# Performance work log

Hardware: AMD Instinct MI355X
Metric: run time of the kernel (lower is better)

Reference implementation:

```python
import jax, jax.numpy as jnp
import numpy as np

B, T, C = 32, 1024, 1024
N_LAYER, LAYER_ID, FIRST_SA = 12, 3, 1
RWKV_K_CLAMP = 60.0
RWKV_K_EPS = 1e-16


def _init_params():
    # decay_speed init exactly as in RWKV_TimeMix.__init__
    f1 = 3.0 + (LAYER_ID - FIRST_SA) / (N_LAYER - 1 - FIRST_SA) * (1.2 - 3.0)
    f2 = 0.65 + (LAYER_ID - FIRST_SA) / (N_LAYER - 1 - FIRST_SA) * (0.4 - 0.65)
    h = np.arange(C, dtype=np.float64)
    decay_speed = np.power(f2, h / (C - 1) * 7) * f1
    time_decay = np.log(decay_speed).astype(np.float32)          # (C,)
    time_first = np.full((C,), np.log(0.3), dtype=np.float32)     # (C,)
    tm = np.ones((C,), dtype=np.float32)
    tm[: C // 2] = 0.0                                            # time_mix
    return jnp.asarray(time_decay), jnp.asarray(time_first), jnp.asarray(tm)


def setup_inputs() -> dict:
    key = jax.random.key(0)
    ks = jax.random.split(key, 5)
    x = jax.random.normal(ks[0], (B, T, C), dtype=jnp.float32)
    scale = 0.02
    Wk = jax.random.normal(ks[1], (C, C), dtype=jnp.float32) * scale
    Wv = jax.random.normal(ks[2], (C, C), dtype=jnp.float32) * scale
    Wr = jax.random.normal(ks[3], (C, C), dtype=jnp.float32) * scale
    Wo = jax.random.normal(ks[4], (C, C), dtype=jnp.float32) * scale
    time_decay, time_first, time_mix = _init_params()
    return {"x": x, "time_decay": time_decay, "time_first": time_first,
            "time_mix": time_mix, "Wk": Wk, "Wv": Wv, "Wr": Wr, "Wo": Wo}


def _wkv(decay, first_w, y, eps):
    # out[b,t,c] = eps + first_w[c]*y[b,t,c] + sum_{u<t} decay[c]^(t-1-u) * y[b,u,c]
    # computed as a linear recurrence S[t] = decay*S[t-1] + y[t] via associative scan.
    a = jnp.broadcast_to(decay, y.shape)
    def comb(l, r):
        a1, b1 = l
        a2, b2 = r
        return (a1 * a2, a2 * b1 + b2)
    _, S = jax.lax.associative_scan(comb, (a, y), axis=1)
    S_prev = jnp.pad(S, ((0, 0), (1, 0), (0, 0)))[:, :-1]  # S[t-1], S[-1]=0
    return eps + first_w * y + S_prev


def reference(x, time_decay, time_first, time_mix, Wk, Wv, Wr, Wo):
    Bn, Tn, Cn = x.shape
    # time shift: ZeroPad2d((0,0,1,-1)) -> shifted[t] = x[t-1], shifted[0]=0
    xs = jnp.pad(x, ((0, 0), (1, 0), (0, 0)))[:, :-1]
    xm = x * time_mix + xs * (1.0 - time_mix)
    k = xm @ Wk.T
    v = xm @ Wv.T
    r = xm @ Wr.T
    k = jnp.exp(jnp.minimum(k, RWKV_K_CLAMP))
    kv = k * v
    decay = jnp.exp(-jnp.exp(time_decay))   # lag-d weight (d>=1): decay^(d-1)
    first_w = jnp.exp(time_first)           # lag-0 weight
    wkv = _wkv(decay, first_w, kv, 0.0)
    wk = _wkv(decay, first_w, k, RWKV_K_EPS)
    rwkv = jax.nn.sigmoid(r) * (wkv / wk)
    return rwkv @ Wo.T
```

## Files before the change

### kernel.cpp

```cpp
#include <hip/hip_runtime.h>


#define DEV __device__ __forceinline__

constexpr int Bc = 32, Tc = 1024, Cc = 1024;
constexpr int Mdim = Bc * Tc;
constexpr int Ndim = Cc;
constexpr int Kdim = Cc;
constexpr int NT = Kdim / 32;
constexpr int CHUNK = 128;
constexpr int LOOKB = 128;
constexpr int NCH = Tc / CHUNK;

typedef short bf16x8 __attribute__((ext_vector_type(8)));
typedef float f32x4  __attribute__((ext_vector_type(4)));

DEV unsigned short f2bf(float f) {
    unsigned u = __float_as_uint(f);
    u += 0x7FFFu + ((u >> 16) & 1u);
    return (unsigned short)(u >> 16);
}
DEV float bf2f(unsigned short s) { return __uint_as_float(((unsigned)s) << 16); }

DEV void gload16(const unsigned short* g, unsigned short* l) {
    __builtin_amdgcn_global_load_lds(
        (const __attribute__((address_space(1))) void*)g,
        (__attribute__((address_space(3))) void*)l, 16, 0, 0);
}

__global__ void wconv_kernel(const float* __restrict__ src, unsigned short* __restrict__ dst) {
    int i = blockIdx.x * blockDim.x + threadIdx.x;
    float4 v = ((const float4*)src)[i];
    ((ushort4*)dst)[i] = make_ushort4(f2bf(v.x), f2bf(v.y), f2bf(v.z), f2bf(v.w));
}

__global__ void xm_kernel(const float* __restrict__ x, const float* __restrict__ tm,
                          unsigned short* __restrict__ xm) {
    int i4 = blockIdx.x * blockDim.x + threadIdx.x;
    int c4 = i4 & (Cc / 4 - 1);
    int t  = (i4 >> 8) & (Tc - 1);
    float4 xc = ((const float4*)x)[i4];
    float4 xp = make_float4(0.f, 0.f, 0.f, 0.f);
    if (t > 0) xp = ((const float4*)x)[i4 - Cc / 4];
    float4 tv = ((const float4*)tm)[c4];
    ushort4 o = make_ushort4(
        f2bf(xc.x * tv.x + xp.x * (1.f - tv.x)),
        f2bf(xc.y * tv.y + xp.y * (1.f - tv.y)),
        f2bf(xc.z * tv.z + xp.z * (1.f - tv.z)),
        f2bf(xc.w * tv.w + xp.w * (1.f - tv.w)));
    ((ushort4*)xm)[i4] = o;
}

template <int MODE>
__global__ __launch_bounds__(512, 1) void gemm256_kernel(
    const unsigned short* __restrict__ A,
    const unsigned short* __restrict__ W,
    void* __restrict__ out)
{
    __shared__ unsigned short lds[3 * 16384];

    const int tid = threadIdx.x;
    const int l = tid & 63, w = tid >> 6;
    const int wr = w >> 2, wc = w & 3;
    const int l15 = l & 15, l4 = l >> 4;
    const size_t row0 = (size_t)blockIdx.x * 256;
    const int col0 = blockIdx.y * 256;

    const int rs = w * 16 + (l >> 2);
    const int cs = ((l & 3) ^ ((l >> 3) & 3)) << 3;
    const int csw = (l4 << 3) ^ (((l15 >> 1) & 3) << 3);

    f32x4 acc[8][4];
#pragma unroll
    for (int m = 0; m < 8; m++)
#pragma unroll
        for (int n = 0; n < 4; n++)
#pragma unroll
            for (int q = 0; q < 4; q++) acc[m][n][q] = 0.f;

#define STAGE_A(kt, bufi) {                                                        \
    _Pragma("unroll")                                                              \
    for (int i = 0; i < 2; i++)                                                    \
        gload16(A + (row0 + i * 128 + rs) * (size_t)Kdim + (kt) * 32 + cs,         \
                lds + (bufi) * 16384 + (i * 512 + w * 64) * 8); }

#define STAGE_B(kt, bufi) {                                                        \
    _Pragma("unroll")                                                              \
    for (int i = 0; i < 2; i++)                                                    \
        gload16(W + (size_t)(col0 + i * 128 + rs) * Kdim + (kt) * 32 + cs,         \
                lds + (bufi) * 16384 + 8192 + (i * 512 + w * 64) * 8); }

    STAGE_A(0, 0); STAGE_B(0, 0); STAGE_A(1, 1); STAGE_B(1, 1);
    asm volatile("s_waitcnt vmcnt(4)" ::: "memory");
    asm volatile("s_barrier" ::: "memory");
    __builtin_amdgcn_sched_barrier(0);

    int buf = 0;
    for (int t = 0; t < NT; t++) {
        int nbuf = buf + 2; if (nbuf >= 3) nbuf -= 3;
        const unsigned short* Ab = lds + buf * 16384;
        const unsigned short* Bb = Ab + 8192;
        bf16x8 af0[4], af1[4], bfr[4];

#pragma unroll
        for (int mi = 0; mi < 4; mi++)
            af0[mi] = *(const bf16x8*)(Ab + (wr * 128 + mi * 16 + l15) * 32 + csw);
#pragma unroll
        for (int n = 0; n < 4; n++)
            bfr[n] = *(const bf16x8*)(Bb + (wc * 64 + n * 16 + l15) * 32 + csw);
        if (t < NT - 2) STAGE_A(t + 2, nbuf);
        asm volatile("s_barrier" ::: "memory");
        __builtin_amdgcn_sched_barrier(0);
        __builtin_amdgcn_s_setprio(1);
#pragma unroll
        for (int mi = 0; mi < 4; mi++)
#pragma unroll
            for (int n = 0; n < 4; n++)
                acc[mi][n] = __builtin_amdgcn_mfma_f32_16x16x32_bf16(af0[mi], bfr[n], acc[mi][n], 0, 0, 0);
        __builtin_amdgcn_s_setprio(0);

#pragma unroll
        for (int mi = 0; mi < 4; mi++)
            af1[mi] = *(const bf16x8*)(Ab + (wr * 128 + (4 + mi) * 16 + l15) * 32 + csw);
        if (t < NT - 2) {
            STAGE_B(t + 2, nbuf);
            asm volatile("s_waitcnt vmcnt(4)" ::: "memory");
        } else if (t == NT - 2) {
            asm volatile("s_waitcnt vmcnt(0)" ::: "memory");
        }
        asm volatile("s_barrier" ::: "memory");
        __builtin_amdgcn_sched_barrier(0);
        __builtin_amdgcn_s_setprio(1);
#pragma unroll
        for (int mi = 0; mi < 4; mi++)
#pragma unroll
            for (int n = 0; n < 4; n++)
                acc[4 + mi][n] = __builtin_amdgcn_mfma_f32_16x16x32_bf16(af1[mi], bfr[n], acc[4 + mi][n], 0, 0, 0);
        __builtin_amdgcn_s_setprio(0);

        buf = buf + 1; if (buf >= 3) buf = 0;
    }

#undef STAGE_A
#undef STAGE_B

#pragma unroll
    for (int m = 0; m < 8; m++)
#pragma unroll
        for (int n = 0; n < 4; n++)
#pragma unroll
            for (int q = 0; q < 4; q++) {
                size_t row = row0 + wr * 128 + m * 16 + l4 * 4 + q;
                int col = col0 + wc * 64 + n * 16 + l15;
                size_t idx = row * Ndim + col;
                float v = acc[m][n][q];
                if constexpr (MODE == 0)
                    ((unsigned short*)out)[idx] = f2bf(__expf(fminf(v, 60.f)));
                else if constexpr (MODE == 1)
                    ((unsigned short*)out)[idx] = f2bf(v);
                else if constexpr (MODE == 2)
                    ((unsigned short*)out)[idx] = f2bf(1.f / (1.f + __expf(-v)));
                else
                    ((float*)out)[idx] = v;
            }
}

__global__ __launch_bounds__(256) void scan_kernel(
    const unsigned short* __restrict__ kexp, const unsigned short* __restrict__ vb,
    const unsigned short* __restrict__ sr,
    const float* __restrict__ td, const float* __restrict__ tf,
    unsigned short* __restrict__ rwkv)
{
    int c = blockIdx.x * blockDim.x + threadIdx.x;
    int ch = blockIdx.y;
    int b  = blockIdx.z;
    int t0 = ch * CHUNK;
    int tstart = t0 - LOOKB; if (tstart < 0) tstart = 0;

    float decay = __expf(-__expf(td[c]));
    float fw = __expf(tf[c]);
    float Skv = 0.f, Sk = 0.f;

    size_t base = (size_t)b * Tc * Cc + c;
    size_t idx = base + (size_t)tstart * Cc;
#pragma unroll 8
    for (int t = tstart; t < t0; t++, idx += Cc) {
        float kk = bf2f(kexp[idx]);
        float y  = kk * bf2f(vb[idx]);
        Skv = decay * Skv + y;
        Sk  = decay * Sk  + kk;
    }
#pragma unroll 8
    for (int t = t0; t < t0 + CHUNK; t++, idx += Cc) {
        float kk = bf2f(kexp[idx]);
        float y  = kk * bf2f(vb[idx]);
        float wkv = fw * y + Skv;
        float wk  = 1e-16f + fw * kk + Sk;
        float sig = bf2f(sr[idx]);
        rwkv[idx] = f2bf(sig * (wkv / wk));
        Skv = decay * Skv + y;
        Sk  = decay * Sk  + kk;
    }
}

extern "C" void kernel_launch(void* const* d_in, const int* in_sizes, int n_in,
                              void* d_out, int out_size, void* d_ws, size_t ws_size,
                              hipStream_t stream) {
    const float* x  = (const float*)d_in[0];
    const float* td = (const float*)d_in[1];
    const float* tf = (const float*)d_in[2];
    const float* tm = (const float*)d_in[3];
    const float* Wk = (const float*)d_in[4];
    const float* Wv = (const float*)d_in[5];
    const float* Wr = (const float*)d_in[6];
    const float* Wo = (const float*)d_in[7];

    const size_t BTC = (size_t)Bc * Tc * Cc;
    const size_t WN  = (size_t)Cc * Cc;

    char* ws = (char*)d_ws;
    unsigned short* wkb   = (unsigned short*)ws; ws += WN * 2;
    unsigned short* wvb   = (unsigned short*)ws; ws += WN * 2;
    unsigned short* wrb   = (unsigned short*)ws; ws += WN * 2;
    unsigned short* wob   = (unsigned short*)ws; ws += WN * 2;
    unsigned short* xm    = (unsigned short*)ws; ws += BTC * 2;
    unsigned short* kexpb = (unsigned short*)ws; ws += BTC * 2;
    unsigned short* vbb   = (unsigned short*)ws; ws += BTC * 2;
    unsigned short* srb   = (unsigned short*)ws; ws += BTC * 2;
    float* outp = (float*)d_out;

    wconv_kernel<<<WN / 1024, 256, 0, stream>>>(Wk, wkb);
    wconv_kernel<<<WN / 1024, 256, 0, stream>>>(Wv, wvb);
    wconv_kernel<<<WN / 1024, 256, 0, stream>>>(Wr, wrb);
    wconv_kernel<<<WN / 1024, 256, 0, stream>>>(Wo, wob);

    xm_kernel<<<BTC / 4 / 256, 256, 0, stream>>>(x, tm, xm);

    dim3 ggrid(Mdim / 256, Ndim / 256);
    gemm256_kernel<0><<<ggrid, 512, 0, stream>>>(xm, wkb, (void*)kexpb);
    gemm256_kernel<1><<<ggrid, 512, 0, stream>>>(xm, wvb, (void*)vbb);
    gemm256_kernel<2><<<ggrid, 512, 0, stream>>>(xm, wrb, (void*)srb);

    scan_kernel<<<dim3(Cc / 256, NCH, Bc), 256, 0, stream>>>(kexpb, vbb, srb, td, tf, xm);

    gemm256_kernel<3><<<ggrid, 512, 0, stream>>>(xm, wob, (void*)outp);
}
```

Before: 450.1 us.

## Restructure GEMM main loop to BK=64 double-buffered with quadrant-split MFMA phases

The bf16 GEMM K-step grows from 32 to 64, the triple-buffered 32-wide LDS ring becomes a double buffer of 64-wide tiles with an XOR-8 swizzle, and each iteration is split into four MFMA quadrant phases separated by barriers. Each phase loads its A/B fragments just before use. The goal is to halve loop-iteration and barrier overhead per unit of K and improve LDS bank behaviour. Launch bounds now ask for 2 blocks per CU, but 128KB of LDS per block likely prevents that. Prefetch depth also drops from two tiles to one, which risks exposing more global-load latency.

After: 447.8 us. Within noise of the previous version (-0.5%).

```diff
diff --git a/kernel.cpp b/kernel.cpp
--- a/kernel.cpp
+++ b/kernel.cpp
@@ -7,7 +7,7 @@
 constexpr int Mdim = Bc * Tc;
 constexpr int Ndim = Cc;
 constexpr int Kdim = Cc;
-constexpr int NT = Kdim / 32;
+constexpr int NT = Kdim / 64;
 constexpr int CHUNK = 128;
 constexpr int LOOKB = 128;
 constexpr int NCH = Tc / CHUNK;
@@ -22,7 +22,7 @@
 }
 DEV float bf2f(unsigned short s) { return __uint_as_float(((unsigned)s) << 16); }
 
-DEV void gload16(const unsigned short* g, unsigned short* l) {
+DEV void gload16(const unsigned short* g, const unsigned short* l) {
     __builtin_amdgcn_global_load_lds(
         (const __attribute__((address_space(1))) void*)g,
         (__attribute__((address_space(3))) void*)l, 16, 0, 0);
@@ -52,12 +52,12 @@
 }
 
 template <int MODE>
-__global__ __launch_bounds__(512, 1) void gemm256_kernel(
+__global__ __launch_bounds__(512, 2) void gemm256_kernel(
     const unsigned short* __restrict__ A,
     const unsigned short* __restrict__ W,
     void* __restrict__ out)
 {
-    __shared__ unsigned short lds[3 * 16384];
+    __shared__ unsigned short lds[2 * 32768];
 
     const int tid = threadIdx.x;
     const int l = tid & 63, w = tid >> 6;
@@ -66,9 +66,9 @@
     const size_t row0 = (size_t)blockIdx.x * 256;
     const int col0 = blockIdx.y * 256;
 
-    const int rs = w * 16 + (l >> 2);
-    const int cs = ((l & 3) ^ ((l >> 3) & 3)) << 3;
-    const int csw = (l4 << 3) ^ (((l15 >> 1) & 3) << 3);
+    const int rs = tid >> 3;
+    const int cs = ((tid & 7) ^ ((tid >> 3) & 7)) << 3;
+    const int swz = (l15 & 7) << 3;
 
     f32x4 acc[8][4];
 #pragma unroll
@@ -78,71 +78,96 @@
 #pragma unroll
             for (int q = 0; q < 4; q++) acc[m][n][q] = 0.f;
 
-#define STAGE_A(kt, bufi) {                                                        \
-    _Pragma("unroll")                                                              \
-    for (int i = 0; i < 2; i++)                                                    \
-        gload16(A + (row0 + i * 128 + rs) * (size_t)Kdim + (kt) * 32 + cs,         \
-                lds + (bufi) * 16384 + (i * 512 + w * 64) * 8); }
-
-#define STAGE_B(kt, bufi) {                                                        \
-    _Pragma("unroll")                                                              \
-    for (int i = 0; i < 2; i++)                                                    \
-        gload16(W + (size_t)(col0 + i * 128 + rs) * Kdim + (kt) * 32 + cs,         \
-                lds + (bufi) * 16384 + 8192 + (i * 512 + w * 64) * 8); }
-
-    STAGE_A(0, 0); STAGE_B(0, 0); STAGE_A(1, 1); STAGE_B(1, 1);
-    asm volatile("s_waitcnt vmcnt(4)" ::: "memory");
-    asm volatile("s_barrier" ::: "memory");
-    __builtin_amdgcn_sched_barrier(0);
-
-    int buf = 0;
+#define STAGE(kt, bb) {                                                                \
+    _Pragma("unroll")                                                                  \
+    for (int g = 0; g < 4; g++)                                                        \
+        gload16(A + (row0 + g * 64 + rs) * (size_t)Kdim + (kt) + cs,                   \
+                lds + (bb) * 32768 + g * 4096 + w * 512);                              \
+    _Pragma("unroll")                                                                  \
+    for (int g = 0; g < 4; g++)                                                        \
+        gload16(W + (size_t)(col0 + g * 64 + rs) * Kdim + (kt) + cs,                   \
+                lds + (bb) * 32768 + 16384 + g * 4096 + w * 512); }
+
+    STAGE(0, 0)
+    asm volatile("s_waitcnt vmcnt(0)" ::: "memory");
+    __builtin_amdgcn_s_barrier();
+
     for (int t = 0; t < NT; t++) {
-        int nbuf = buf + 2; if (nbuf >= 3) nbuf -= 3;
-        const unsigned short* Ab = lds + buf * 16384;
-        const unsigned short* Bb = Ab + 8192;
-        bf16x8 af0[4], af1[4], bfr[4];
-
-#pragma unroll
-        for (int mi = 0; mi < 4; mi++)
-            af0[mi] = *(const bf16x8*)(Ab + (wr * 128 + mi * 16 + l15) * 32 + csw);
-#pragma unroll
-        for (int n = 0; n < 4; n++)
-            bfr[n] = *(const bf16x8*)(Bb + (wc * 64 + n * 16 + l15) * 32 + csw);
-        if (t < NT - 2) STAGE_A(t + 2, nbuf);
-        asm volatile("s_barrier" ::: "memory");
-        __builtin_amdgcn_sched_barrier(0);
-        __builtin_amdgcn_s_setprio(1);
-#pragma unroll
-        for (int mi = 0; mi < 4; mi++)
-#pragma unroll
-            for (int n = 0; n < 4; n++)
-                acc[mi][n] = __builtin_amdgcn_mfma_f32_16x16x32_bf16(af0[mi], bfr[n], acc[mi][n], 0, 0, 0);
-        __builtin_amdgcn_s_setprio(0);
-
-#pragma unroll
-        for (int mi = 0; mi < 4; mi++)
-            af1[mi] = *(const bf16x8*)(Ab + (wr * 128 + (4 + mi) * 16 + l15) * 32 + csw);
-        if (t < NT - 2) {
-            STAGE_B(t + 2, nbuf);
-            asm volatile("s_waitcnt vmcnt(4)" ::: "memory");
-        } else if (t == NT - 2) {
-            asm volatile("s_waitcnt vmcnt(0)" ::: "memory");
-        }
-        asm volatile("s_barrier" ::: "memory");
-        __builtin_amdgcn_sched_barrier(0);
-        __builtin_amdgcn_s_setprio(1);
-#pragma unroll
-        for (int mi = 0; mi < 4; mi++)
-#pragma unroll
-            for (int n = 0; n < 4; n++)
-                acc[4 + mi][n] = __builtin_amdgcn_mfma_f32_16x16x32_bf16(af1[mi], bfr[n], acc[4 + mi][n], 0, 0, 0);
-        __builtin_amdgcn_s_setprio(0);
-
-        buf = buf + 1; if (buf >= 3) buf = 0;
+        const int b = t & 1;
+        const unsigned short* Ab = lds + b * 32768;
+        const unsigned short* Bb = Ab + 16384;
+        bf16x8 af0[4][2], af1[4][2], bf0[2][2], bf1[2][2];
+
+#pragma unroll
+        for (int mi = 0; mi < 4; mi++)
+#pragma unroll
+            for (int kk = 0; kk < 2; kk++)
+                af0[mi][kk] = *(const bf16x8*)(Ab + (wr * 128 + mi * 16 + l15) * 64 + ((kk * 32 + l4 * 8) ^ swz));
+#pragma unroll
+        for (int n = 0; n < 2; n++)
+#pragma unroll
+            for (int kk = 0; kk < 2; kk++)
+                bf0[n][kk] = *(const bf16x8*)(Bb + (wc * 64 + n * 16 + l15) * 64 + ((kk * 32 + l4 * 8) ^ swz));
+        if (t < NT - 1) STAGE((t + 1) * 64, b ^ 1)
+        __builtin_amdgcn_s_barrier();
+        asm volatile("s_waitcnt lgkmcnt(0)" ::: "memory");
+        __builtin_amdgcn_s_setprio(1);
+#pragma unroll
+        for (int mi = 0; mi < 4; mi++)
+#pragma unroll
+            for (int n = 0; n < 2; n++)
+#pragma unroll
+                for (int kk = 0; kk < 2; kk++)
+                    acc[mi][n] = __builtin_amdgcn_mfma_f32_16x16x32_bf16(af0[mi][kk], bf0[n][kk], acc[mi][n], 0, 0, 0);
+        __builtin_amdgcn_s_setprio(0);
+
+#pragma unroll
+        for (int n = 0; n < 2; n++)
+#pragma unroll
+            for (int kk = 0; kk < 2; kk++)
+                bf1[n][kk] = *(const bf16x8*)(Bb + (wc * 64 + (2 + n) * 16 + l15) * 64 + ((kk * 32 + l4 * 8) ^ swz));
+        __builtin_amdgcn_s_barrier();
+        asm volatile("s_waitcnt lgkmcnt(0)" ::: "memory");
+        __builtin_amdgcn_s_setprio(1);
+#pragma unroll
+        for (int mi = 0; mi < 4; mi++)
+#pragma unroll
+            for (int n = 0; n < 2; n++)
+#pragma unroll
+                for (int kk = 0; kk < 2; kk++)
+                    acc[mi][2 + n] = __builtin_amdgcn_mfma_f32_16x16x32_bf16(af0[mi][kk], bf1[n][kk], acc[mi][2 + n], 0, 0, 0);
+        __builtin_amdgcn_s_setprio(0);
+
+#pragma unroll
+        for (int mi = 0; mi < 4; mi++)
+#pragma unroll
+            for (int kk = 0; kk < 2; kk++)
+                af1[mi][kk] = *(const bf16x8*)(Ab + (wr * 128 + (4 + mi) * 16 + l15) * 64 + ((kk * 32 + l4 * 8) ^ swz));
+        __builtin_amdgcn_s_barrier();
+        asm volatile("s_waitcnt lgkmcnt(0)" ::: "memory");
+        __builtin_amdgcn_s_setprio(1);
+#pragma unroll
+        for (int mi = 0; mi < 4; mi++)
+#pragma unroll
+            for (int n = 0; n < 2; n++)
+#pragma unroll
+                for (int kk = 0; kk < 2; kk++)
+                    acc[4 + mi][n] = __builtin_amdgcn_mfma_f32_16x16x32_bf16(af1[mi][kk], bf0[n][kk], acc[4 + mi][n], 0, 0, 0);
+        __builtin_amdgcn_s_setprio(0);
+
+        if (t < NT - 1) { asm volatile("s_waitcnt vmcnt(0)" ::: "memory"); }
+        __builtin_amdgcn_s_barrier();
+        __builtin_amdgcn_s_setprio(1);
+#pragma unroll
+        for (int mi = 0; mi < 4; mi++)
+#pragma unroll
+            for (int n = 0; n < 2; n++)
+#pragma unroll
+                for (int kk = 0; kk < 2; kk++)
+                    acc[4 + mi][2 + n] = __builtin_amdgcn_mfma_f32_16x16x32_bf16(af1[mi][kk], bf1[n][kk], acc[4 + mi][2 + n], 0, 0, 0);
+        __builtin_amdgcn_s_setprio(0);
     }
-
-#undef STAGE_A
-#undef STAGE_B
+#undef STAGE
 
 #pragma unroll
     for (int m = 0; m < 8; m++)
```

## Fuse K/V/R projections into one GEMM launch with a four-stage LDS pipeline

Applied to the files above, without the earlier changes.

The three separate K, V and R projection GEMMs become a single launch over a 12-column-block grid. It relies on the bf16 Wk, Wv and Wr buffers sitting back to back in the workspace, so they act as one 3072-row weight matrix. Each block picks its epilogue (exp-clamp, plain, or sigmoid) from blockIdx.y. The main loop also moves from a 3-buffer to a 4-buffer global-to-LDS pipeline with three tiles in flight, adds extra barriers and lgkmcnt waits, and raises launch_bounds to 2 blocks per CU. Intended gains are fewer launches, a better wave tail and deeper latency hiding. The 128KB LDS tile may still allow only one block per CU, and the tighter register budget risks spills.

Measured after the change: 469.3 us. 1.04x slower.

```diff
diff --git a/kernel.cpp b/kernel.cpp
--- a/kernel.cpp
+++ b/kernel.cpp
@@ -7,7 +7,7 @@
 constexpr int Mdim = Bc * Tc;
 constexpr int Ndim = Cc;
 constexpr int Kdim = Cc;
-constexpr int NT = Kdim / 32;
+constexpr int NH = Kdim / 32;
 constexpr int CHUNK = 128;
 constexpr int LOOKB = 128;
 constexpr int NCH = Tc / CHUNK;
@@ -22,7 +22,7 @@
 }
 DEV float bf2f(unsigned short s) { return __uint_as_float(((unsigned)s) << 16); }
 
-DEV void gload16(const unsigned short* g, unsigned short* l) {
+DEV void gload16(const unsigned short* g, const unsigned short* l) {
     __builtin_amdgcn_global_load_lds(
         (const __attribute__((address_space(1))) void*)g,
         (__attribute__((address_space(3))) void*)l, 16, 0, 0);
@@ -51,24 +51,27 @@
     ((ushort4*)xm)[i4] = o;
 }
 
-template <int MODE>
-__global__ __launch_bounds__(512, 1) void gemm256_kernel(
+template <int FUSED>
+__global__ __launch_bounds__(512, 2) void gemm256_kernel(
     const unsigned short* __restrict__ A,
     const unsigned short* __restrict__ W,
-    void* __restrict__ out)
+    unsigned short* __restrict__ ok,
+    unsigned short* __restrict__ ov,
+    unsigned short* __restrict__ orr,
+    float* __restrict__ of)
 {
-    __shared__ unsigned short lds[3 * 16384];
+    __shared__ unsigned short lds[65536];
 
     const int tid = threadIdx.x;
     const int l = tid & 63, w = tid >> 6;
     const int wr = w >> 2, wc = w & 3;
     const int l15 = l & 15, l4 = l >> 4;
     const size_t row0 = (size_t)blockIdx.x * 256;
-    const int col0 = blockIdx.y * 256;
-
-    const int rs = w * 16 + (l >> 2);
-    const int cs = ((l & 3) ^ ((l >> 3) & 3)) << 3;
-    const int csw = (l4 << 3) ^ (((l15 >> 1) & 3) << 3);
+    const int ncol0 = blockIdx.y * 256;
+
+    const int rs = tid >> 2;
+    const int cs = ((tid & 3) ^ ((tid >> 3) & 3)) << 3;
+    const int csw = (l4 ^ ((l15 >> 1) & 3)) << 3;
 
     f32x4 acc[8][4];
 #pragma unroll
@@ -78,72 +81,68 @@
 #pragma unroll
             for (int q = 0; q < 4; q++) acc[m][n][q] = 0.f;
 
-#define STAGE_A(kt, bufi) {                                                        \
-    _Pragma("unroll")                                                              \
-    for (int i = 0; i < 2; i++)                                                    \
-        gload16(A + (row0 + i * 128 + rs) * (size_t)Kdim + (kt) * 32 + cs,         \
-                lds + (bufi) * 16384 + (i * 512 + w * 64) * 8); }
-
-#define STAGE_B(kt, bufi) {                                                        \
-    _Pragma("unroll")                                                              \
-    for (int i = 0; i < 2; i++)                                                    \
-        gload16(W + (size_t)(col0 + i * 128 + rs) * Kdim + (kt) * 32 + cs,         \
-                lds + (bufi) * 16384 + 8192 + (i * 512 + w * 64) * 8); }
-
-    STAGE_A(0, 0); STAGE_B(0, 0); STAGE_A(1, 1); STAGE_B(1, 1);
-    asm volatile("s_waitcnt vmcnt(4)" ::: "memory");
+#define STAGE_AH(hh) {                                                                  \
+    _Pragma("unroll")                                                                   \
+    for (int g = 0; g < 2; g++)                                                         \
+        gload16(A + (row0 + g * 128 + rs) * (size_t)Kdim + (hh) * 32 + cs,              \
+                lds + ((hh) & 3) * 16384 + g * 4096 + w * 512); }
+#define STAGE_BH(hh) {                                                                  \
+    _Pragma("unroll")                                                                   \
+    for (int g = 0; g < 2; g++)                                                         \
+        gload16(W + (size_t)(ncol0 + g * 128 + rs) * Kdim + (hh) * 32 + cs,             \
+                lds + ((hh) & 3) * 16384 + 8192 + g * 4096 + w * 512); }
+
+    STAGE_AH(0) STAGE_BH(0) STAGE_AH(1) STAGE_BH(1) STAGE_AH(2) STAGE_BH(2)
+    asm volatile("s_waitcnt vmcnt(8)" ::: "memory");
     asm volatile("s_barrier" ::: "memory");
-    __builtin_amdgcn_sched_barrier(0);
-
-    int buf = 0;
-    for (int t = 0; t < NT; t++) {
-        int nbuf = buf + 2; if (nbuf >= 3) nbuf -= 3;
-        const unsigned short* Ab = lds + buf * 16384;
+
+    for (int h = 0; h < NH; h++) {
+        const unsigned short* Ab = lds + (h & 3) * 16384;
         const unsigned short* Bb = Ab + 8192;
-        bf16x8 af0[4], af1[4], bfr[4];
-
-#pragma unroll
-        for (int mi = 0; mi < 4; mi++)
-            af0[mi] = *(const bf16x8*)(Ab + (wr * 128 + mi * 16 + l15) * 32 + csw);
+        bf16x8 af[4], bfr[4];
+
+#pragma unroll
+        for (int mi = 0; mi < 4; mi++)
+            af[mi] = *(const bf16x8*)(Ab + (wr * 128 + mi * 16 + l15) * 32 + csw);
 #pragma unroll
         for (int n = 0; n < 4; n++)
             bfr[n] = *(const bf16x8*)(Bb + (wc * 64 + n * 16 + l15) * 32 + csw);
-        if (t < NT - 2) STAGE_A(t + 2, nbuf);
-        asm volatile("s_barrier" ::: "memory");
+        if (h + 3 < NH) STAGE_AH(h + 3)
+        asm volatile("s_barrier" ::: "memory");
+        asm volatile("s_waitcnt lgkmcnt(0)" ::: "memory");
         __builtin_amdgcn_sched_barrier(0);
         __builtin_amdgcn_s_setprio(1);
 #pragma unroll
         for (int mi = 0; mi < 4; mi++)
 #pragma unroll
             for (int n = 0; n < 4; n++)
-                acc[mi][n] = __builtin_amdgcn_mfma_f32_16x16x32_bf16(af0[mi], bfr[n], acc[mi][n], 0, 0, 0);
+                acc[mi][n] = __builtin_amdgcn_mfma_f32_16x16x32_bf16(af[mi], bfr[n], acc[mi][n], 0, 0, 0);
         __builtin_amdgcn_s_setprio(0);
-
-#pragma unroll
-        for (int mi = 0; mi < 4; mi++)
-            af1[mi] = *(const bf16x8*)(Ab + (wr * 128 + (4 + mi) * 16 + l15) * 32 + csw);
-        if (t < NT - 2) {
-            STAGE_B(t + 2, nbuf);
-            asm volatile("s_waitcnt vmcnt(4)" ::: "memory");
-        } else if (t == NT - 2) {
-            asm volatile("s_waitcnt vmcnt(0)" ::: "memory");
-        }
-        asm volatile("s_barrier" ::: "memory");
+        asm volatile("s_barrier" ::: "memory");
+
+#pragma unroll
+        for (int mi = 0; mi < 4; mi++)
+            af[mi] = *(const bf16x8*)(Ab + (wr * 128 + (4 + mi) * 16 + l15) * 32 + csw);
+        if (h + 3 < NH) STAGE_BH(h + 3)
+        if (h < NH - 3) { asm volatile("s_waitcnt vmcnt(8)" ::: "memory"); }
+        else           { asm volatile("s_waitcnt vmcnt(0)" ::: "memory"); }
+        asm volatile("s_barrier" ::: "memory");
+        asm volatile("s_waitcnt lgkmcnt(0)" ::: "memory");
         __builtin_amdgcn_sched_barrier(0);
         __builtin_amdgcn_s_setprio(1);
 #pragma unroll
         for (int mi = 0; mi < 4; mi++)
 #pragma unroll
             for (int n = 0; n < 4; n++)
-                acc[4 + mi][n] = __builtin_amdgcn_mfma_f32_16x16x32_bf16(af1[mi], bfr[n], acc[4 + mi][n], 0, 0, 0);
+                acc[4 + mi][n] = __builtin_amdgcn_mfma_f32_16x16x32_bf16(af[mi], bfr[n], acc[4 + mi][n], 0, 0, 0);
         __builtin_amdgcn_s_setprio(0);
-
-        buf = buf + 1; if (buf >= 3) buf = 0;
+        asm volatile("s_barrier" ::: "memory");
     }
-
-#undef STAGE_A
-#undef STAGE_B
-
+#undef STAGE_AH
+#undef STAGE_BH
+
+    const int mode = FUSED ? (blockIdx.y >> 2) : 3;
+    const int colb = FUSED ? ((blockIdx.y & 3) * 256) : ncol0;
 #pragma unroll
     for (int m = 0; m < 8; m++)
 #pragma unroll
@@ -151,17 +150,16 @@
 #pragma unroll
             for (int q = 0; q < 4; q++) {
                 size_t row = row0 + wr * 128 + m * 16 + l4 * 4 + q;
-                int col = col0 + wc * 64 + n * 16 + l15;
+                int col = colb + wc * 64 + n * 16 + l15;
                 size_t idx = row * Ndim + col;
                 float v = acc[m][n][q];
-                if constexpr (MODE == 0)
-                    ((unsigned short*)out)[idx] = f2bf(__expf(fminf(v, 60.f)));
-                else if constexpr (MODE == 1)
-                    ((unsigned short*)out)[idx] = f2bf(v);
-                else if constexpr (MODE == 2)
-                    ((unsigned short*)out)[idx] = f2bf(1.f / (1.f + __expf(-v)));
-                else
-                    ((float*)out)[idx] = v;
+                if (FUSED) {
+                    if (mode == 0)      ok[idx]  = f2bf(__expf(fminf(v, 60.f)));
+                    else if (mode == 1) ov[idx]  = f2bf(v);
+                    else                orr[idx] = f2bf(1.f / (1.f + __expf(-v)));
+                } else {
+                    of[idx] = v;
+                }
             }
 }
 
@@ -236,12 +234,11 @@
 
     xm_kernel<<<BTC / 4 / 256, 256, 0, stream>>>(x, tm, xm);
 
-    dim3 ggrid(Mdim / 256, Ndim / 256);
-    gemm256_kernel<0><<<ggrid, 512, 0, stream>>>(xm, wkb, (void*)kexpb);
-    gemm256_kernel<1><<<ggrid, 512, 0, stream>>>(xm, wvb, (void*)vbb);
-    gemm256_kernel<2><<<ggrid, 512, 0, stream>>>(xm, wrb, (void*)srb);
+    gemm256_kernel<1><<<dim3(Mdim / 256, 12), 512, 0, stream>>>(
+        xm, wkb, kexpb, vbb, srb, nullptr);
 
     scan_kernel<<<dim3(Cc / 256, NCH, Bc), 256, 0, stream>>>(kexpb, vbb, srb, td, tf, xm);
 
-    gemm256_kernel<3><<<ggrid, 512, 0, stream>>>(xm, wob, (void*)outp);
-}
+    gemm256_kernel<0><<<dim3(Mdim / 256, 4), 512, 0, stream>>>(
+        xm, wob, nullptr, nullptr, nullptr, outp);
+}
```
